# Kernel tuning notes

Measured on AMD Instinct MI355X. Metric: run time of the kernel, lower is better.

## Reference

```python
import jax, jax.numpy as jnp
import numpy as np

N = 50000

def sage_conv(x, edge_index, W_l, b_l, W_r):
    # PyG SAGEConv (aggr='mean'): out = lin_l(mean_{j in N(i)} x_j) + lin_r(x_i)
    src, dst = edge_index[0], edge_index[1]
    msg = x[src]                                            # [E, d]
    summed = jax.ops.segment_sum(msg, dst, num_segments=N)  # [N, d]
    deg = jax.ops.segment_sum(jnp.ones((edge_index.shape[1],), x.dtype), dst, num_segments=N)
    agg = summed / jnp.maximum(deg, 1.0)[:, None]
    return agg @ W_l.T + b_l + x @ W_r.T

def setup_inputs() -> dict:
    key = jax.random.key(0)
    ks = jax.random.split(key, 8)
    in_c, hid_c, out_c, E = 128, 256, 128, 800000
    x = jax.random.normal(ks[0], (N, in_c), dtype=jnp.float32)
    edge_index = jax.random.randint(ks[1], (2, E), 0, N, dtype=jnp.int64)
    s = lambda k, shp, fan: jax.random.normal(k, shp, jnp.float32) * (1.0 / np.sqrt(fan))
    return {
        "x": x,
        "edge_index": edge_index,
        "W1_l": s(ks[2], (hid_c, in_c), in_c),
        "b1": jnp.zeros((hid_c,), jnp.float32),
        "W1_r": s(ks[3], (hid_c, in_c), in_c),
        "W2_l": s(ks[4], (out_c, hid_c), hid_c),
        "b2": jnp.zeros((out_c,), jnp.float32),
        "W2_r": s(ks[5], (out_c, hid_c), hid_c),
    }

def reference(x, edge_index, W1_l, b1, W1_r, W2_l, b2, W2_r):
    h = jax.nn.relu(sage_conv(x, edge_index, W1_l, b1, W1_r))
    # dropout is identity in eval mode
    return sage_conv(h, edge_index, W2_l, b2, W2_r)
```

## Files before the change

### kernel.cpp

```cpp
#include <hip/hip_runtime.h>
#include <hip/hip_bf16.h>


typedef short short8 __attribute__((ext_vector_type(8)));
typedef float floatx4 __attribute__((ext_vector_type(4)));

#define IN_C  128
#define HID_C 256
#define OUT_C 128
#define NBMAX 400
#define CHUNK 3072
#define CAP   2560
#define NBIN  261
#define NCAST 200
#define NWPK  56

static __device__ __forceinline__ unsigned short f2b(float f) {
  union { float f; unsigned u; } v; v.f = f;
  unsigned r = v.u + 0x7fffu + ((v.u >> 16) & 1u);
  return (unsigned short)(r >> 16);
}
static __device__ __forceinline__ unsigned pack2(float a, float b) {
  return (unsigned)f2b(a) | ((unsigned)f2b(b) << 16);
}
static __device__ __forceinline__ float lo2f(unsigned u) {
  union { unsigned u; float f; } v; v.u = u << 16; return v.f;
}
static __device__ __forceinline__ float hi2f(unsigned u) {
  union { unsigned u; float f; } v; v.u = u & 0xffff0000u; return v.f;
}


__global__ void __launch_bounds__(512)
k_binprep(const int* __restrict__ ei, int E, int nb,
          int* __restrict__ cursor, unsigned* __restrict__ staged,
          const float* __restrict__ x, unsigned* __restrict__ xb, int nPairsX,
          const float* __restrict__ W1l, const float* __restrict__ W1r,
          const float* __restrict__ W2l, const float* __restrict__ W2r,
          unsigned* __restrict__ wpk1, unsigned* __restrict__ wpk2) {
  __shared__ unsigned sbuf[CHUNK];
  __shared__ int lh[512];
  __shared__ int loff[NBMAX];
  __shared__ int lcnt[NBMAX];
  __shared__ int lcur[NBMAX];
  __shared__ int gb[NBMAX];
  __shared__ int wsum[8];
  int blk = blockIdx.x, tid = threadIdx.x;

  if (blk >= NBIN) {
    if (blk < NBIN + NCAST) {
      for (int i = (blk - NBIN) * 512 + tid; i < nPairsX; i += NCAST * 512) {
        float2 v = reinterpret_cast<const float2*>(x)[i];
        xb[i] = pack2(v.x, v.y);
      }
    } else {
      for (int i = (blk - NBIN - NCAST) * 512 + tid; i < 65536; i += NWPK * 512) {
        int j = i & 32767;
        int u = j & 3;
        int lane = (j >> 2) & 63;
        int kk = (j >> 8) & 7;
        int g = j >> 11;
        int n = g * 16 + (lane & 15);
        int kc = kk * 4 + (lane >> 4);
        int pc = kc * 4 + u;
        if (i < 32768) {
          const float* s = (pc < 64) ? (W1l + (size_t)n * 128 + pc * 2)
                                     : (W1r + (size_t)n * 128 + (pc - 64) * 2);
          float2 v = *reinterpret_cast<const float2*>(s);
          wpk1[j] = pack2(v.x, v.y);
        } else {
          const float* s = (n < 128) ? (W2l + (size_t)n * 256 + pc * 2)
                                     : (W2r + (size_t)(n - 128) * 256 + pc * 2);
          float2 v = *reinterpret_cast<const float2*>(s);
          wpk2[j] = pack2(v.x, v.y);
        }
      }
    }
    return;
  }

  int lane = tid & 63, wv = tid >> 6;
  int e0 = blk * CHUNK;
  int e1 = min(e0 + CHUNK, E);
  lh[tid] = 0;
  __syncthreads();
  for (int e = e0 + tid; e < e1; e += 512)
    atomicAdd(&lh[((unsigned)ei[E + e]) >> 7], 1);
  __syncthreads();
  int v = lh[tid];
  int s = v;
#pragma unroll
  for (int off = 1; off < 64; off <<= 1) {
    int t = __shfl_up(s, off, 64);
    if (lane >= off) s += t;
  }
  if (lane == 63) wsum[wv] = s;
  __syncthreads();
  if (wv == 0 && lane < 8) {
    int t = wsum[lane];
#pragma unroll
    for (int off = 1; off < 8; off <<= 1) {
      int u = __shfl_up(t, off, 64);
      if (lane >= off) t += u;
    }
    wsum[lane] = t;
  }
  __syncthreads();
  int woff = (wv == 0) ? 0 : wsum[wv - 1];
  int excl = woff + s - v;
  if (tid < nb) {
    loff[tid] = excl; lcnt[tid] = v; lcur[tid] = excl;
    gb[tid] = tid * CAP + atomicAdd(&cursor[tid], v);
  }
  __syncthreads();
  for (int e = e0 + tid; e < e1; e += 512) {
    int dst = ei[E + e];
    int src = ei[e];
    int b = ((unsigned)dst) >> 7;
    int p = atomicAdd(&lcur[b], 1);
    sbuf[p] = ((unsigned)src << 7) | (unsigned)(dst & 127);
  }
  __syncthreads();
  for (int b = wv; b < nb; b += 8) {
    int lbeg = loff[b], cnt = lcnt[b], gbase = gb[b];
    for (int p = lane; p < cnt; p += 64)
      staged[gbase + p] = sbuf[lbeg + p];
  }
}


__global__ void k_csr(const unsigned* __restrict__ staged, const int* __restrict__ cursor,
                      int2* __restrict__ offs2, int* __restrict__ srcs, int N) {
  __shared__ int cnt[128];
  __shared__ int cur[128];
  int b = blockIdx.x;
  int tid = threadIdx.x;
  int gbeg = b * CAP, gend = gbeg + cursor[b];
  if (tid < 128) cnt[tid] = 0;
  __syncthreads();
  for (int j = gbeg + tid; j < gend; j += 256)
    atomicAdd(&cnt[staged[j] & 127], 1);
  __syncthreads();
  if (tid < 64) {
    int v0 = cnt[tid * 2], v1 = cnt[tid * 2 + 1];
    int s = v0 + v1;
#pragma unroll
    for (int off = 1; off < 64; off <<= 1) {
      int t = __shfl_up(s, off, 64);
      if (tid >= off) s += t;
    }
    int exclp = s - (v0 + v1);
    int node = b * 128 + tid * 2;
    int beg0 = gbeg + exclp;
    int beg1 = beg0 + v0;
    cur[tid * 2]     = beg0;
    cur[tid * 2 + 1] = beg1;
    if (node < N)     offs2[node]     = make_int2(beg0, beg1);
    if (node + 1 < N) offs2[node + 1] = make_int2(beg1, beg1 + v1);
  }
  __syncthreads();
  for (int j = gbeg + tid; j < gend; j += 256) {
    unsigned v = staged[j];
    int pos = atomicAdd(&cur[v & 127], 1);
    srcs[pos] = (int)(v >> 7);
  }
}


static __device__ __forceinline__ void acc8(float* s, uint4 p) {
  s[0] += lo2f(p.x); s[1] += hi2f(p.x);
  s[2] += lo2f(p.y); s[3] += hi2f(p.y);
  s[4] += lo2f(p.z); s[5] += hi2f(p.z);
  s[6] += lo2f(p.w); s[7] += hi2f(p.w);
}

__global__ void k_agg_store(const uint4* __restrict__ Z4,
                            const int2* __restrict__ offs2, const int* __restrict__ srcs,
                            uint4* __restrict__ out4, int N) {
  int node = blockIdx.x * 4 + (threadIdx.x >> 6);
  if (node >= N) return;
  int lane = threadIdx.x & 63;
  int g = lane >> 4, c = lane & 15;
  int2 be = offs2[node];
  int beg = be.x, end = be.y;
  float s[8] = {};
  int j = beg;
  for (; j + 16 <= end; j += 16) {
    uint4 p0 = Z4[(size_t)srcs[j +      g] * 16 + c];
    uint4 p1 = Z4[(size_t)srcs[j +  4 + g] * 16 + c];
    uint4 p2 = Z4[(size_t)srcs[j +  8 + g] * 16 + c];
    uint4 p3 = Z4[(size_t)srcs[j + 12 + g] * 16 + c];
    acc8(s, p0); acc8(s, p1); acc8(s, p2); acc8(s, p3);
  }
  for (; j + 4 <= end; j += 4) {
    uint4 p = Z4[(size_t)srcs[j + g] * 16 + c];
    acc8(s, p);
  }
  if (j + g < end) {
    uint4 p = Z4[(size_t)srcs[j + g] * 16 + c];
    acc8(s, p);
  }
#pragma unroll
  for (int i = 0; i < 8; ++i) {
    s[i] += __shfl_xor(s[i], 16);
    s[i] += __shfl_xor(s[i], 32);
  }
  if (g == 0) {
    int d = end - beg;
    float inv = 1.0f / (float)(d > 0 ? d : 1);
    uint4 o;
    o.x = pack2(s[0] * inv, s[1] * inv);
    o.y = pack2(s[2] * inv, s[3] * inv);
    o.z = pack2(s[4] * inv, s[5] * inv);
    o.w = pack2(s[6] * inv, s[7] * inv);
    out4[(size_t)node * 16 + c] = o;
  }
}

__global__ void k_agg_addout(const uint4* __restrict__ Z4,
                             const int2* __restrict__ offs2, const int* __restrict__ srcs,
                             const uint4* __restrict__ Bb4,
                             float* __restrict__ Out, int N) {
  int node = blockIdx.x * 4 + (threadIdx.x >> 6);
  if (node >= N) return;
  int lane = threadIdx.x & 63;
  int g = lane >> 4, c = lane & 15;
  int2 be = offs2[node];
  int beg = be.x, end = be.y;
  float s[8] = {};
  int j = beg;
  for (; j + 16 <= end; j += 16) {
    uint4 p0 = Z4[(size_t)srcs[j +      g] * 16 + c];
    uint4 p1 = Z4[(size_t)srcs[j +  4 + g] * 16 + c];
    uint4 p2 = Z4[(size_t)srcs[j +  8 + g] * 16 + c];
    uint4 p3 = Z4[(size_t)srcs[j + 12 + g] * 16 + c];
    acc8(s, p0); acc8(s, p1); acc8(s, p2); acc8(s, p3);
  }
  for (; j + 4 <= end; j += 4) {
    uint4 p = Z4[(size_t)srcs[j + g] * 16 + c];
    acc8(s, p);
  }
  if (j + g < end) {
    uint4 p = Z4[(size_t)srcs[j + g] * 16 + c];
    acc8(s, p);
  }
#pragma unroll
  for (int i = 0; i < 8; ++i) {
    s[i] += __shfl_xor(s[i], 16);
    s[i] += __shfl_xor(s[i], 32);
  }
  if (g == 0) {
    int d = end - beg;
    float inv = 1.0f / (float)(d > 0 ? d : 1);
    uint4 bp = Bb4[(size_t)node * 16 + c];
    float4 o0, o1;
    o0.x = lo2f(bp.x) + s[0] * inv; o0.y = hi2f(bp.x) + s[1] * inv;
    o0.z = lo2f(bp.y) + s[2] * inv; o0.w = hi2f(bp.y) + s[3] * inv;
    o1.x = lo2f(bp.z) + s[4] * inv; o1.y = hi2f(bp.z) + s[5] * inv;
    o1.z = lo2f(bp.w) + s[6] * inv; o1.w = hi2f(bp.w) + s[7] * inv;
    float* op = Out + (size_t)node * 128 + c * 8;
    *reinterpret_cast<float4*>(op) = o0;
    *reinterpret_cast<float4*>(op + 4) = o1;
  }
}


static __device__ __forceinline__ void stage_dual(
    const unsigned short* A1, const unsigned short* A2, int mBase,
    unsigned short* At ) {
  int t = threadIdx.x;
#pragma unroll
  for (int it = 0; it < 8; ++it) {
    int q = it * 256 + t;
    int r = q >> 5;
    int p = q & 31;
    int d = (p & 16) | ((p ^ r) & 15);
    const unsigned short* g = (d < 16)
        ? (A1 + (size_t)(mBase + r) * 128 + d * 8)
        : (A2 + (size_t)(mBase + r) * 128 + (d - 16) * 8);
    __builtin_amdgcn_global_load_lds(
        (const __attribute__((address_space(1))) unsigned*)g,
        (__attribute__((address_space(3))) unsigned*)&At[q * 8], 16, 0, 0);
  }
}

__global__ void __launch_bounds__(256, 3)
k_gemm12(const unsigned short* __restrict__ A1, const unsigned short* __restrict__ A2,
         const unsigned short* __restrict__ Wpk1, const float* __restrict__ b1,
         const unsigned short* __restrict__ Wpk2, const float* __restrict__ b2,
         unsigned short* __restrict__ Zb, unsigned short* __restrict__ Bb, int M) {
  __shared__ unsigned short At[64 * 256];
  int mBase = blockIdx.x * 64;
  stage_dual(A1, A2, mBase, At);
  int lane = threadIdx.x & 63, wave = threadIdx.x >> 6;
  int l15 = lane & 15, quad = lane >> 4;
  const short8* Wf1 = reinterpret_cast<const short8*>(Wpk1);
  const short8* Wf2 = reinterpret_cast<const short8*>(Wpk2);

  floatx4 acc[4][4] = {};
  __syncthreads();
#pragma unroll 2
  for (int kk = 0; kk < 8; ++kk) {
    short8 b[4];
#pragma unroll
    for (int t = 0; t < 4; ++t)
      b[t] = Wf1[((wave * 4 + t) * 8 + kk) * 64 + lane];
    int kc = kk * 4 + quad;
#pragma unroll
    for (int s = 0; s < 4; ++s) {
      int row = s * 16 + l15;
      int pos = (kc & 16) | ((kc ^ row) & 15);
      short8 a = *reinterpret_cast<const short8*>(&At[row * 256 + pos * 8]);
#pragma unroll
      for (int t = 0; t < 4; ++t)
        acc[s][t] = __builtin_amdgcn_mfma_f32_16x16x32_bf16(a, b[t], acc[s][t], 0, 0, 0);
    }
  }
  __syncthreads();

#pragma unroll
  for (int t = 0; t < 4; ++t) {
    int n = wave * 64 + t * 16 + l15;
    float bv = b1[n];
    int d = n >> 3, nl = n & 7;
#pragma unroll
    for (int s = 0; s < 4; ++s) {
#pragma unroll
      for (int r = 0; r < 4; ++r) {
        int m = s * 16 + quad * 4 + r;
        int pos = (d & 16) | ((d ^ m) & 15);
        At[m * 256 + pos * 8 + nl] = f2b(fmaxf(acc[s][t][r] + bv, 0.f));
      }
    }
  }
#pragma unroll
  for (int s = 0; s < 4; ++s)
#pragma unroll
    for (int t = 0; t < 4; ++t)
      acc[s][t] = floatx4{0.f, 0.f, 0.f, 0.f};
  __syncthreads();

#pragma unroll 2
  for (int kk = 0; kk < 8; ++kk) {
    short8 b[4];
#pragma unroll
    for (int t = 0; t < 4; ++t)
      b[t] = Wf2[((wave * 4 + t) * 8 + kk) * 64 + lane];
    int kc = kk * 4 + quad;
#pragma unroll
    for (int s = 0; s < 4; ++s) {
      int row = s * 16 + l15;
      int pos = (kc & 16) | ((kc ^ row) & 15);
      short8 a = *reinterpret_cast<const short8*>(&At[row * 256 + pos * 8]);
#pragma unroll
      for (int t = 0; t < 4; ++t)
        acc[s][t] = __builtin_amdgcn_mfma_f32_16x16x32_bf16(a, b[t], acc[s][t], 0, 0, 0);
    }
  }
  if (wave < 2) {
#pragma unroll
    for (int t = 0; t < 4; ++t) {
      int n = wave * 64 + t * 16 + l15;
#pragma unroll
      for (int s = 0; s < 4; ++s)
#pragma unroll
        for (int r = 0; r < 4; ++r) {
          int m = mBase + s * 16 + quad * 4 + r;
          if (m < M) Zb[(size_t)m * 128 + n] = f2b(acc[s][t][r]);
        }
    }
  } else {
#pragma unroll
    for (int t = 0; t < 4; ++t) {
      int n = (wave - 2) * 64 + t * 16 + l15;
      float bv = b2[n];
#pragma unroll
      for (int s = 0; s < 4; ++s)
#pragma unroll
        for (int r = 0; r < 4; ++r) {
          int m = mBase + s * 16 + quad * 4 + r;
          if (m < M) Bb[(size_t)m * 128 + n] = f2b(acc[s][t][r] + bv);
        }
    }
  }
}


extern "C" void kernel_launch(void* const* d_in, const int* in_sizes, int n_in,
                              void* d_out, int out_size, void* d_ws, size_t ws_size,
                              hipStream_t stream) {
  const float* x   = (const float*)d_in[0];
  const int*   ei  = (const int*)d_in[1];
  const float* W1l = (const float*)d_in[2];
  const float* b1  = (const float*)d_in[3];
  const float* W1r = (const float*)d_in[4];
  const float* W2l = (const float*)d_in[5];
  const float* b2  = (const float*)d_in[6];
  const float* W2r = (const float*)d_in[7];
  float* out = (float*)d_out;

  int N = in_sizes[0] / IN_C;
  int E = in_sizes[1] / 2;
  int nb = (N + 127) >> 7;

  char* p = (char*)d_ws;
  auto alloc = [&](size_t bytes) -> void* {
    void* r = (void*)p;
    p += (bytes + 255) & ~(size_t)255;
    return r;
  };
  int* cursor  = (int*)alloc((size_t)(nb + 1) * 4);
  unsigned* staged = (unsigned*)alloc((size_t)nb * CAP * 4);
  int2* offs2 = (int2*)alloc((size_t)N * 8);
  int* srcs   = (int*)alloc((size_t)nb * CAP * 4);
  unsigned* xb   = (unsigned*)alloc((size_t)N * IN_C * 2);
  unsigned* agg1 = (unsigned*)alloc((size_t)N * IN_C * 2);
  unsigned short* zb = (unsigned short*)alloc((size_t)N * OUT_C * 2);
  unsigned short* baseb = (unsigned short*)alloc((size_t)N * OUT_C * 2);
  unsigned* wpk1 = (unsigned*)alloc((size_t)HID_C * 256 * 2);
  unsigned* wpk2 = (unsigned*)alloc((size_t)256 * HID_C * 2);
  (void)alloc(64 * 512);

  hipMemsetAsync(cursor, 0, (size_t)(nb + 1) * 4, stream);
  k_binprep<<<NBIN + NCAST + NWPK, 512, 0, stream>>>(
      ei, E, nb, cursor, staged, x, xb, N * IN_C / 2,
      W1l, W1r, W2l, W2r, wpk1, wpk2);
  k_csr<<<nb, 256, 0, stream>>>(staged, cursor, offs2, srcs, N);

  int mBlocks = (N + 63) / 64;

  k_agg_store<<<(N + 3) / 4, 256, 0, stream>>>(
      (const uint4*)xb, offs2, srcs, (uint4*)agg1, N);
  k_gemm12<<<mBlocks, 256, 0, stream>>>(
      (const unsigned short*)agg1, (const unsigned short*)xb,
      (const unsigned short*)wpk1, b1,
      (const unsigned short*)wpk2, b2, zb, baseb, N);

  k_agg_addout<<<(N + 3) / 4, 256, 0, stream>>>(
      (const uint4*)zb, offs2, srcs, (const uint4*)baseb, out, N);
}
```

Measured before the change: 202.9 us.

## Fuse first-layer mean aggregation into the dual GEMM kernel via shared memory

Removes the separate k_agg_store kernel and the agg1 global buffer. Each GEMM block now gathers and averages neighbour features for its 64 rows directly into a swizzled LDS tile, split into separate aggregate and self-feature halves. This saves a global write and re-read of the aggregated tensor plus one launch. In exchange the gather now runs inside a GEMM block with limited occupancy (launch bounds 256,3, only 782 blocks), so latency hiding for the irregular gathers may be worse than in the standalone high-parallelism kernel.

```diff
diff --git a/kernel.cpp b/kernel.cpp
--- a/kernel.cpp
+++ b/kernel.cpp
@@ -174,49 +174,6 @@
   s[6] += lo2f(p.w); s[7] += hi2f(p.w);
 }
 
-__global__ void k_agg_store(const uint4* __restrict__ Z4,
-                            const int2* __restrict__ offs2, const int* __restrict__ srcs,
-                            uint4* __restrict__ out4, int N) {
-  int node = blockIdx.x * 4 + (threadIdx.x >> 6);
-  if (node >= N) return;
-  int lane = threadIdx.x & 63;
-  int g = lane >> 4, c = lane & 15;
-  int2 be = offs2[node];
-  int beg = be.x, end = be.y;
-  float s[8] = {};
-  int j = beg;
-  for (; j + 16 <= end; j += 16) {
-    uint4 p0 = Z4[(size_t)srcs[j +      g] * 16 + c];
-    uint4 p1 = Z4[(size_t)srcs[j +  4 + g] * 16 + c];
-    uint4 p2 = Z4[(size_t)srcs[j +  8 + g] * 16 + c];
-    uint4 p3 = Z4[(size_t)srcs[j + 12 + g] * 16 + c];
-    acc8(s, p0); acc8(s, p1); acc8(s, p2); acc8(s, p3);
-  }
-  for (; j + 4 <= end; j += 4) {
-    uint4 p = Z4[(size_t)srcs[j + g] * 16 + c];
-    acc8(s, p);
-  }
-  if (j + g < end) {
-    uint4 p = Z4[(size_t)srcs[j + g] * 16 + c];
-    acc8(s, p);
-  }
-#pragma unroll
-  for (int i = 0; i < 8; ++i) {
-    s[i] += __shfl_xor(s[i], 16);
-    s[i] += __shfl_xor(s[i], 32);
-  }
-  if (g == 0) {
-    int d = end - beg;
-    float inv = 1.0f / (float)(d > 0 ? d : 1);
-    uint4 o;
-    o.x = pack2(s[0] * inv, s[1] * inv);
-    o.y = pack2(s[2] * inv, s[3] * inv);
-    o.z = pack2(s[4] * inv, s[5] * inv);
-    o.w = pack2(s[6] * inv, s[7] * inv);
-    out4[(size_t)node * 16 + c] = o;
-  }
-}
-
 __global__ void k_agg_addout(const uint4* __restrict__ Z4,
                              const int2* __restrict__ offs2, const int* __restrict__ srcs,
                              const uint4* __restrict__ Bb4,
@@ -265,35 +222,71 @@
 }
 
 
-static __device__ __forceinline__ void stage_dual(
-    const unsigned short* A1, const unsigned short* A2, int mBase,
-    unsigned short* At ) {
-  int t = threadIdx.x;
-#pragma unroll
-  for (int it = 0; it < 8; ++it) {
-    int q = it * 256 + t;
-    int r = q >> 5;
-    int p = q & 31;
-    int d = (p & 16) | ((p ^ r) & 15);
-    const unsigned short* g = (d < 16)
-        ? (A1 + (size_t)(mBase + r) * 128 + d * 8)
-        : (A2 + (size_t)(mBase + r) * 128 + (d - 16) * 8);
-    __builtin_amdgcn_global_load_lds(
-        (const __attribute__((address_space(1))) unsigned*)g,
-        (__attribute__((address_space(3))) unsigned*)&At[q * 8], 16, 0, 0);
-  }
-}
-
 __global__ void __launch_bounds__(256, 3)
-k_gemm12(const unsigned short* __restrict__ A1, const unsigned short* __restrict__ A2,
+k_gemm12(const unsigned short* __restrict__ Xb, const uint4* __restrict__ Xb4,
+         const int2* __restrict__ offs2, const int* __restrict__ srcs,
          const unsigned short* __restrict__ Wpk1, const float* __restrict__ b1,
          const unsigned short* __restrict__ Wpk2, const float* __restrict__ b2,
          unsigned short* __restrict__ Zb, unsigned short* __restrict__ Bb, int M) {
-  __shared__ unsigned short At[64 * 256];
+  __shared__ unsigned short Aag[64 * 128];
+  __shared__ unsigned short Axb[64 * 128];
   int mBase = blockIdx.x * 64;
-  stage_dual(A1, A2, mBase, At);
-  int lane = threadIdx.x & 63, wave = threadIdx.x >> 6;
+  int tid = threadIdx.x;
+  int lane = tid & 63, wave = tid >> 6;
   int l15 = lane & 15, quad = lane >> 4;
+
+#pragma unroll
+  for (int it = 0; it < 4; ++it) {
+    int q = it * 256 + tid;
+    int r = q >> 4;
+    int pp = q & 15;
+    int c = (pp ^ r) & 15;
+    const unsigned short* g = Xb + (size_t)(mBase + r) * 128 + c * 8;
+    __builtin_amdgcn_global_load_lds(
+        (const __attribute__((address_space(1))) unsigned*)g,
+        (__attribute__((address_space(3))) unsigned*)&Axb[q * 8], 16, 0, 0);
+  }
+
+  for (int i = 0; i < 16; ++i) {
+    int r = wave * 16 + i;
+    int node = mBase + r;
+    int g = lane >> 4, c = l15;
+    int beg = 0, end = 0;
+    if (node < M) { int2 be = offs2[node]; beg = be.x; end = be.y; }
+    float s[8] = {};
+    int j = beg;
+    for (; j + 16 <= end; j += 16) {
+      uint4 p0 = Xb4[(size_t)srcs[j +      g] * 16 + c];
+      uint4 p1 = Xb4[(size_t)srcs[j +  4 + g] * 16 + c];
+      uint4 p2 = Xb4[(size_t)srcs[j +  8 + g] * 16 + c];
+      uint4 p3 = Xb4[(size_t)srcs[j + 12 + g] * 16 + c];
+      acc8(s, p0); acc8(s, p1); acc8(s, p2); acc8(s, p3);
+    }
+    for (; j + 4 <= end; j += 4) {
+      uint4 p = Xb4[(size_t)srcs[j + g] * 16 + c];
+      acc8(s, p);
+    }
+    if (j + g < end) {
+      uint4 p = Xb4[(size_t)srcs[j + g] * 16 + c];
+      acc8(s, p);
+    }
+#pragma unroll
+    for (int b = 0; b < 8; ++b) {
+      s[b] += __shfl_xor(s[b], 16);
+      s[b] += __shfl_xor(s[b], 32);
+    }
+    if (lane < 16) {
+      int d = end - beg;
+      float inv = 1.0f / (float)(d > 0 ? d : 1);
+      uint4 o;
+      o.x = pack2(s[0] * inv, s[1] * inv);
+      o.y = pack2(s[2] * inv, s[3] * inv);
+      o.z = pack2(s[4] * inv, s[5] * inv);
+      o.w = pack2(s[6] * inv, s[7] * inv);
+      *reinterpret_cast<uint4*>(&Aag[r * 128 + ((c ^ r) & 15) * 8]) = o;
+    }
+  }
+
   const short8* Wf1 = reinterpret_cast<const short8*>(Wpk1);
   const short8* Wf2 = reinterpret_cast<const short8*>(Wpk2);
 
@@ -306,11 +299,12 @@
     for (int t = 0; t < 4; ++t)
       b[t] = Wf1[((wave * 4 + t) * 8 + kk) * 64 + lane];
     int kc = kk * 4 + quad;
+    const unsigned short* Ah = (kc < 16) ? Aag : Axb;
+    int kl = kc & 15;
 #pragma unroll
     for (int s = 0; s < 4; ++s) {
       int row = s * 16 + l15;
-      int pos = (kc & 16) | ((kc ^ row) & 15);
-      short8 a = *reinterpret_cast<const short8*>(&At[row * 256 + pos * 8]);
+      short8 a = *reinterpret_cast<const short8*>(&Ah[row * 128 + ((kl ^ row) & 15) * 8]);
 #pragma unroll
       for (int t = 0; t < 4; ++t)
         acc[s][t] = __builtin_amdgcn_mfma_f32_16x16x32_bf16(a, b[t], acc[s][t], 0, 0, 0);
@@ -323,13 +317,14 @@
     int n = wave * 64 + t * 16 + l15;
     float bv = b1[n];
     int d = n >> 3, nl = n & 7;
+    unsigned short* Hh = (d < 16) ? Aag : Axb;
+    int dl = d & 15;
 #pragma unroll
     for (int s = 0; s < 4; ++s) {
 #pragma unroll
       for (int r = 0; r < 4; ++r) {
         int m = s * 16 + quad * 4 + r;
-        int pos = (d & 16) | ((d ^ m) & 15);
-        At[m * 256 + pos * 8 + nl] = f2b(fmaxf(acc[s][t][r] + bv, 0.f));
+        Hh[m * 128 + ((dl ^ m) & 15) * 8 + nl] = f2b(fmaxf(acc[s][t][r] + bv, 0.f));
       }
     }
   }
@@ -347,11 +342,12 @@
     for (int t = 0; t < 4; ++t)
       b[t] = Wf2[((wave * 4 + t) * 8 + kk) * 64 + lane];
     int kc = kk * 4 + quad;
+    const unsigned short* Ah = (kc < 16) ? Aag : Axb;
+    int kl = kc & 15;
 #pragma unroll
     for (int s = 0; s < 4; ++s) {
       int row = s * 16 + l15;
-      int pos = (kc & 16) | ((kc ^ row) & 15);
-      short8 a = *reinterpret_cast<const short8*>(&At[row * 256 + pos * 8]);
+      short8 a = *reinterpret_cast<const short8*>(&Ah[row * 128 + ((kl ^ row) & 15) * 8]);
 #pragma unroll
       for (int t = 0; t < 4; ++t)
         acc[s][t] = __builtin_amdgcn_mfma_f32_16x16x32_bf16(a, b[t], acc[s][t], 0, 0, 0);
@@ -414,7 +410,6 @@
   int2* offs2 = (int2*)alloc((size_t)N * 8);
   int* srcs   = (int*)alloc((size_t)nb * CAP * 4);
   unsigned* xb   = (unsigned*)alloc((size_t)N * IN_C * 2);
-  unsigned* agg1 = (unsigned*)alloc((size_t)N * IN_C * 2);
   unsigned short* zb = (unsigned short*)alloc((size_t)N * OUT_C * 2);
   unsigned short* baseb = (unsigned short*)alloc((size_t)N * OUT_C * 2);
   unsigned* wpk1 = (unsigned*)alloc((size_t)HID_C * 256 * 2);
@@ -429,10 +424,8 @@
 
   int mBlocks = (N + 63) / 64;
 
-  k_agg_store<<<(N + 3) / 4, 256, 0, stream>>>(
-      (const uint4*)xb, offs2, srcs, (uint4*)agg1, N);
   k_gemm12<<<mBlocks, 256, 0, stream>>>(
-      (const unsigned short*)agg1, (const unsigned short*)xb,
+      (const unsigned short*)xb, (const uint4*)xb, offs2, srcs,
       (const unsigned short*)wpk1, b1,
       (const unsigned short*)wpk2, b2, zb, baseb, N);
 
```

After: 215.8 us. 6.4% more time.
